# Kernel tuning notes

Measured on AMD Instinct MI355X. Metric: run time of the kernel, lower is better.

Reference implementation:

```python
import jax, jax.numpy as jnp
import numpy as np
from jax import lax

B, T, MELS, H, K = 32, 2048, 80, 128, 5
MAX_WORDS, MAX_DUR = 64, 128


def _conv1d(x, w, b):
    # x: [B,C,T], w: [O,I,K]
    y = lax.conv_general_dilated(x, w, (1,), 'SAME',
                                 dimension_numbers=('NCH', 'OIH', 'NCH'))
    return y + b[None, :, None]


def _conv2d(x, w, b):
    # x: [B,C,H,W], w: [O,I,K,K]
    y = lax.conv_general_dilated(x, w, (1, 1), 'SAME',
                                 dimension_numbers=('NCHW', 'OIHW', 'NCHW'))
    return y + b[None, :, None, None]


def setup_inputs() -> dict:
    key = jax.random.key(0)
    ks = jax.random.split(key, 20)
    features = jax.random.normal(ks[0], (B, MELS, T), dtype=jnp.float32)
    # monotone word boundaries in [0, T]; starts = bnds[:, :-1], ends = bnds[:, 1:]
    bnds = jnp.sort(jax.random.randint(ks[1], (B, MAX_WORDS + 1), 0, T), axis=-1)
    word_bounds = jnp.stack([bnds[:, :-1], bnds[:, 1:]], axis=1).astype(jnp.int64)  # [B,2,W]
    word_lengths = jax.random.randint(ks[2], (B,), MAX_WORDS // 2, MAX_WORDS + 1).astype(jnp.int64)
    s = 0.05
    p = {
        'w1': jax.random.normal(ks[3], (H, MELS, K)) * s, 'b1': jnp.zeros((H,)),
        'w2': jax.random.normal(ks[4], (H, H, K)) * s, 'b2': jnp.zeros((H,)),
        'w3': jax.random.normal(ks[5], (H, H, K)) * s, 'b3': jnp.zeros((H,)),
        'cw1': jax.random.normal(ks[6], (H, H, K, K)) * s, 'cb1': jnp.zeros((H,)),
        'cw2': jax.random.normal(ks[7], (H, H, K, K)) * s, 'cb2': jnp.zeros((H,)),
        'lw': jax.random.normal(ks[8], (1, MAX_DUR)) * s, 'lb': jnp.zeros((1,)),
        'cw3': jax.random.normal(ks[9], (1, H, K, K)) * s, 'cb3': jnp.zeros((1,)),
    }
    return {'features': features, 'word_bounds': word_bounds, 'word_lengths': word_lengths, **p}


def _slice_words(emb, word_bounds, word_lengths):
    # emb: [B,H,T] -> padded [B,H,MAX_WORDS,MAX_DUR]
    starts = word_bounds[:, 0, :]                      # [B,W]
    durs = word_bounds[:, 1, :] - starts               # [B,W]
    j = jnp.arange(MAX_DUR)                            # [D]
    idx = starts[:, :, None] + j[None, None, :]        # [B,W,D]
    valid = (j[None, None, :] < durs[:, :, None]) & \
            (jnp.arange(MAX_WORDS)[None, :, None] < word_lengths[:, None, None])
    idx = jnp.clip(idx, 0, emb.shape[-1] - 1)
    gathered = jax.vmap(lambda e, ix: e[:, ix])(emb, idx)  # [B,H,W,D]
    return gathered * valid[:, None, :, :].astype(emb.dtype)


def reference(features, word_bounds, word_lengths,
              w1, b1, w2, b2, w3, b3,
              cw1, cb1, cw2, cb2, lw, lb, cw3, cb3):
    # frame encoder
    x = jax.nn.relu(_conv1d(features, w1, b1))
    x = jax.nn.relu(_conv1d(x, w2, b2))
    emb = _conv1d(x, w3, b3)                           # [B,H,T]
    # ragged word slicing + zero-pad scatter (vectorized gather)
    padded = _slice_words(emb, word_bounds, word_lengths)  # [B,H,W,D]
    # word decoder
    y = jax.nn.relu(_conv2d(padded, cw1, cb1))
    y = jax.nn.relu(_conv2d(y, cw2, cb2))
    y = jax.nn.relu(jnp.einsum('bcwd,od->bcwo', y, lw) + lb)  # Linear over duration dim
    out = _conv2d(y, cw3, cb3)                         # [B,1,W,1]
    return out
```

## Files before the change

kernel.cpp:

```cpp
#include <hip/hip_runtime.h>
#include <hip/hip_bf16.h>

#define BB 32
#define TT 2048
#define MELS 80
#define HH 128
#define WW 64
#define DD 128

using bf16x8 = __attribute__((ext_vector_type(8))) short;
using f32x16 = __attribute__((ext_vector_type(16))) float;
using u16x4  = __attribute__((ext_vector_type(4))) ushort;

#define MFMA(av, bv, acc) acc = __builtin_amdgcn_mfma_f32_32x32x16_bf16(av, bv, acc, 0, 0, 0)

__device__ __forceinline__ ushort bf16b(float f) {
  __hip_bfloat16 h = __float2bfloat16(f);
  return *(ushort*)&h;
}

__device__ __forceinline__ void g2l16(const ushort* g, ushort* l) {
  __builtin_amdgcn_global_load_lds((const __attribute__((address_space(1))) void*)g,
                                   (__attribute__((address_space(3))) void*)l, 16, 0, 0);
}

__device__ __forceinline__ void dump_tile(const f32x16& a, int tl, int mb, int half,
                                          const float* __restrict__ bias, bool relu,
                                          ushort* s_y) {
  #pragma unroll
  for (int q = 0; q < 4; ++q) {
    int ho0 = mb + 8 * q + 4 * half;
    u16x4 p;
    #pragma unroll
    for (int j = 0; j < 4; ++j) {
      float v = a[q * 4 + j] + bias[ho0 + j];
      if (relu) v = fmaxf(v, 0.f);
      p[j] = bf16b(v);
    }
    *(u16x4*)&s_y[tl * 128 + (((ho0 >> 3) ^ (tl & 15)) << 3) + (ho0 & 7)] = p;
  }
}

__global__ __launch_bounds__(256) void prep_all(
    const float* __restrict__ features,
    const float* __restrict__ w1, const float* __restrict__ w2,
    const float* __restrict__ w3, const float* __restrict__ cw1,
    const float* __restrict__ cw2, const float* __restrict__ cb1,
    const float* __restrict__ lw,
    ushort* __restrict__ ft, ushort* __restrict__ Wb1, ushort* __restrict__ Wb2,
    ushort* __restrict__ Wb3, ushort* __restrict__ Wc1, ushort* __restrict__ Wc2,
    float* __restrict__ T2, float* __restrict__ Ls, ushort* __restrict__ zp) {
  __shared__ float s[MELS][65];
  const int bb = blockIdx.x, tid = threadIdx.x;
  if (bb < 1024) {
    const int b = bb >> 5, t0 = (bb & 31) * 64;
    for (int i = tid; i < MELS * 64; i += 256) {
      int c = i >> 6, t = i & 63;
      s[c][t] = features[(b * MELS + c) * TT + t0 + t];
    }
    __syncthreads();
    for (int i = tid; i < 64 * 128; i += 256) {
      int t = i >> 7, c = i & 127;
      float v = (c < MELS) ? s[c][t] : 0.f;
      ft[(b * TT + t0 + t) * 128 + c] = bf16b(v);
    }
  } else if (bb < 1864) {
    int rel, NSS, C; const float* w; ushort* Wb;
    if (bb < 1224)      { rel = bb - 1024; NSS = 5; C = MELS; w = w1; Wb = Wb1; }
    else if (bb < 1544) { rel = bb - 1224; NSS = 8; C = HH;   w = w2; Wb = Wb2; }
    else                { rel = bb - 1544; NSS = 8; C = HH;   w = w3; Wb = Wb3; }
    int i = rel * 256 + tid;
    int e = i & 7, m = (i >> 3) & 127, half = (i >> 10) & 1;
    int r = i >> 11;
    int ss = r % NSS, kw = r / NSS;
    int c = ss * 16 + half * 8 + e;
    Wb[i] = bf16b(w[(m * C + c) * 5 + kw]);
  } else if (bb < 5064) {
    int rel; const float* cw; ushort* Wc;
    if (bb < 3464) { rel = bb - 1864; cw = cw1; Wc = Wc1; }
    else           { rel = bb - 3464; cw = cw2; Wc = Wc2; }
    int i = rel * 256 + tid;
    int e = i & 7, m = (i >> 3) & 127, half = (i >> 10) & 1, ss = (i >> 11) & 7;
    int r = i >> 14;
    int kw = r % 5, kd = r / 5;
    int hi = ss * 16 + half * 8 + e;
    Wc[i] = bf16b(cw[((m * HH + hi) * 5 + kw) * 5 + kd]);
  } else if (bb < 5067) {
    int i = (bb - 5064) * 256 + tid;
    if (i < 640) {
      int ho = i / 5, kw = i - ho * 5;
      float sA = 0.f, sB = 0.f, sC = 0.f;
      for (int hi = 0; hi < HH; ++hi) {
        float yc = fmaxf(cb1[hi], 0.f);
        const float* p = cw2 + ((ho * HH + hi) * 5 + kw) * 5;
        float c012 = p[0] + p[1] + p[2];
        sC += c012 * yc;
        sB += (c012 + p[3]) * yc;
        sA += (c012 + p[3] + p[4]) * yc;
      }
      T2[i * 3 + 0] = sA; T2[i * 3 + 1] = sB; T2[i * 3 + 2] = sC;
    } else if (i < 645) {
      int c = i - 640;
      float sv = 0.f;
      for (int d = c * 32; d < 128; ++d) sv += lw[d];
      Ls[c] = sv;
    }
  } else {
    *(bf16x8*)(zp + tid * 8) = (short)0;
  }
}

template<int NSS, int RELU>
__global__ __launch_bounds__(256) void conv1d_mfma(
    const ushort* __restrict__ xt, const ushort* __restrict__ Wb,
    const float* __restrict__ bias, ushort* __restrict__ yt,
    const ushort* __restrict__ zp) {
  __shared__ __align__(16) ushort s_x[1088 * 8];
  const int bid = blockIdx.x;
  const int nid = (bid & 7) * 128 + (bid >> 3);
  const int b = nid >> 5;
  const int t0 = (nid & 31) << 6;
  const int tid = threadIdx.x;
  const int lane = tid & 63, wv = tid >> 6;
  const int l31 = lane & 31, half = lane >> 5;
  const int m_w = (wv >> 1) * 64, n32 = (wv & 1) * 32;

  #pragma unroll
  for (int it = 0; it < 5; ++it) {
    int slot = it * 256 + tid;
    if (slot < 1088) {
      int row = slot >> 4, bsw = (slot & 15) ^ (row & 15);
      int t = t0 + row - 2;
      const ushort* src = ((unsigned)t < TT)
          ? xt + (((size_t)(b * TT + t)) << 7) + bsw * 8 : zp;
      g2l16(src, s_x + slot * 8);
    }
  }
  __syncthreads();

  f32x16 a0 = 0.f, a1 = 0.f;
  const bf16x8* Ap = (const bf16x8*)Wb;
  constexpr int G = 5 * NSS;
  #pragma unroll
  for (int g = 0; g < G; ++g) {
    const int kw = g / NSS, ss = g % NSS;
    int r0 = n32 + l31 + kw;
    int blk = ss * 2 + half;
    bf16x8 bv = *(const bf16x8*)&s_x[r0 * 128 + ((blk ^ (r0 & 15)) << 3)];
    int ai = ((kw * NSS + ss) * 2 + half) * 128 + m_w + l31;
    MFMA(Ap[ai],      bv, a0);
    MFMA(Ap[ai + 32], bv, a1);
  }
  __syncthreads();
  dump_tile(a0, n32 + l31, m_w,      half, bias, RELU != 0, s_x);
  dump_tile(a1, n32 + l31, m_w + 32, half, bias, RELU != 0, s_x);
  __syncthreads();
  #pragma unroll
  for (int it = 0; it < 4; ++it) {
    int i = it * 256 + tid;
    int tl = i >> 4, blk = i & 15;
    bf16x8 v = *(const bf16x8*)&s_x[tl * 128 + ((blk ^ (tl & 15)) << 3)];
    *(bf16x8*)(yt + (((size_t)(b * TT + t0 + tl)) << 7) + blk * 8) = v;
  }
}

#define COMPUTE2D(KW, BUF, NB)                                                 \
  {                                                                            \
    bf16x8 ar[2][8];                                                           \
    _Pragma("unroll")                                                          \
    for (int j = 0; j < 8; ++j)                                                \
      ar[0][j] = Ap[(((0 * 5 + (KW)) * 8 + (j >> 1)) * 2 + half) * 128 +       \
                    m_w + l31 + (j & 1) * 32];                                 \
    __builtin_amdgcn_s_setprio(1);                                             \
    _Pragma("unroll")                                                          \
    for (int g = 0; g < 10; ++g) {                                             \
      int kd = g >> 1, sh = (g & 1) * 4;                                       \
      if (g < 9) {                                                             \
        int kd2 = (g + 1) >> 1, sh2 = ((g + 1) & 1) * 4;                       \
        _Pragma("unroll")                                                      \
        for (int j = 0; j < 8; ++j)                                            \
          ar[(g + 1) & 1][j] = Ap[(((kd2 * 5 + (KW)) * 8 + sh2 + (j >> 1)) * 2 \
                                   + half) * 128 + m_w + l31 + (j & 1) * 32];  \
      }                                                                        \
      _Pragma("unroll")                                                        \
      for (int s2 = 0; s2 < 4; ++s2) {                                         \
        int ss = sh + s2;                                                      \
        int r0 = n_w + l31 + kd;                                               \
        int blk = ss * 2 + half;                                               \
        bf16x8 bv0 = *(const bf16x8*)&(BUF)[r0 * 128 + ((blk ^ (r0 & 15)) << 3)]; \
        MFMA(ar[g & 1][s2 * 2],     bv0, a00);                                 \
        MFMA(ar[g & 1][s2 * 2 + 1], bv0, a10);                                 \
        if ((NB) > 1) {                                                        \
          int r1 = r0 + 32;                                                    \
          bf16x8 bv1 = *(const bf16x8*)&(BUF)[r1 * 128 + ((blk ^ (r1 & 15)) << 3)]; \
          MFMA(ar[g & 1][s2 * 2],     bv1, a01);                               \
          MFMA(ar[g & 1][s2 * 2 + 1], bv1, a11);                               \
        }                                                                      \
      }                                                                        \
    }                                                                          \
    __builtin_amdgcn_s_setprio(0);                                             \
  }

__global__ __launch_bounds__(256, 4) void conv2d1_mfma(
    const ushort* __restrict__ embt, const int* __restrict__ wb,
    const int* __restrict__ wlen, const ushort* __restrict__ Wc,
    const float* __restrict__ cb, ushort* __restrict__ y1t,
    const ushort* __restrict__ zp) {
  extern __shared__ __align__(16) ushort smem[];
  const int bid = blockIdx.x;
  const int nid = (bid & 7) * 256 + (bid >> 3);
  const int b = nid >> 6, w = nid & 63;
  const int tid = threadIdx.x;
  const int lane = tid & 63, wv = tid >> 6;
  const int l31 = lane & 31, half = lane >> 5;
  const int m_w = (wv >> 1) * 64, n_w = (wv & 1) * 64;

  int stv[5], duv[5];
  const int wl = wlen[b];
  #pragma unroll
  for (int i = 0; i < 5; ++i) {
    int wq = w + i - 2;
    bool ok = ((unsigned)wq < WW) && (wq < wl);
    int st = ok ? wb[b * 128 + wq] : 0;
    int en = ok ? wb[b * 128 + 64 + wq] : 0;
    stv[i] = st;
    duv[i] = ok ? min(en - st, 128) : 0;
  }
  int dcap = 0;
  #pragma unroll
  for (int i = 0; i < 5; ++i) dcap = max(dcap, duv[i]);
  const int NT1 = min(4, max(1, (dcap + 2 + 31) >> 5));
  const int rstage = min(132, NT1 * 32 + 4);
  const int t0a = n_w >> 5;
  const bool act0 = t0a < NT1, act1 = t0a + 1 < NT1;

#define STAGE1(KW)                                                             \
  {                                                                            \
    const int st_ = stv[KW], du_ = duv[KW];                                    \
    if (du_ > 0) {                                                             \
      const int rs_ = min(rstage, (((du_ + 33) >> 5) << 5) + 4);               \
      _Pragma("unroll")                                                        \
      for (int it = 0; it < 9; ++it) {                                         \
        int slot = it * 256 + tid;                                             \
        if (slot < 2112) {                                                     \
          int row = slot >> 4;                                                 \
          if (row < rs_) {                                                     \
            int bsw = (slot & 15) ^ (row & 15);                                \
            int dq = row - 2;                                                  \
            const ushort* src = ((unsigned)dq < (unsigned)du_)                 \
                ? embt + (((size_t)(b * TT + st_ + dq)) << 7) + bsw * 8 : zp;  \
            g2l16(src, smem + slot * 8);                                       \
          }                                                                    \
        }                                                                      \
      }                                                                        \
    }                                                                          \
  }

  f32x16 a00 = 0.f, a01 = 0.f, a10 = 0.f, a11 = 0.f;
  const bf16x8* Ap = (const bf16x8*)Wc;

  STAGE1(0);
  __syncthreads();
  #pragma unroll
  for (int kw = 0; kw < 5; ++kw) {
    const int du = duv[kw];
    const bool a1k = act1 && (du + 2 > n_w + 32);
    const bool a0k = act0 && (du > 0) && (du + 2 > n_w);
    if (a1k)      { COMPUTE2D(kw, smem, 2); }
    else if (a0k) { COMPUTE2D(kw, smem, 1); }
    __syncthreads();
    if (kw < 4) {
      switch (kw + 1) {
        case 1: STAGE1(1); break;
        case 2: STAGE1(2); break;
        case 3: STAGE1(3); break;
        case 4: STAGE1(4); break;
      }
      __syncthreads();
    }
  }
#undef STAGE1

  if (act0) {
    dump_tile(a00, n_w + l31, m_w,      half, cb, true, smem);
    dump_tile(a10, n_w + l31, m_w + 32, half, cb, true, smem);
  }
  if (act1) {
    dump_tile(a01, n_w + 32 + l31, m_w,      half, cb, true, smem);
    dump_tile(a11, n_w + 32 + l31, m_w + 32, half, cb, true, smem);
  }
  __syncthreads();
  bf16x8 cv;
  {
    int blkc = tid & 15;
    #pragma unroll
    for (int j = 0; j < 8; ++j)
      ((ushort*)&cv)[j] = bf16b(fmaxf(cb[blkc * 8 + j], 0.f));
  }
  #pragma unroll
  for (int it = 0; it < 8; ++it) {
    int i = it * 256 + tid;
    int d = i >> 4, blk = i & 15;
    bf16x8 v = (d < NT1 * 32)
        ? *(const bf16x8*)&smem[d * 128 + ((blk ^ (d & 15)) << 3)] : cv;
    *(bf16x8*)(y1t + (((size_t)(b * WW + w) * DD + d) << 7) + blk * 8) = v;
  }
}

__global__ __launch_bounds__(256, 4) void conv2d2_mfma(
    const ushort* __restrict__ y1t, const int* __restrict__ wb,
    const int* __restrict__ wlen, const ushort* __restrict__ Wc,
    const float* __restrict__ cb, const float* __restrict__ lw,
    const float* __restrict__ lb, const float* __restrict__ T2,
    const float* __restrict__ Ls, float* __restrict__ z,
    const ushort* __restrict__ zp) {
  extern __shared__ __align__(16) ushort smem[];
  const int bid = blockIdx.x;
  const int nid = (bid & 7) * 256 + (bid >> 3);
  const int b = nid >> 6, w = nid & 63;
  const int tid = threadIdx.x;
  const int lane = tid & 63, wv = tid >> 6;
  const int l31 = lane & 31, half = lane >> 5;
  const int m_w = (wv >> 1) * 64, n_w = (wv & 1) * 64;

  int dmax = 0;
  const int wl = wlen[b];
  #pragma unroll
  for (int i = 0; i < 9; ++i) {
    int wq = w + i - 4;
    if ((unsigned)wq < WW && wq < wl) {
      int du = min(wb[b * 128 + 64 + wq] - wb[b * 128 + wq], 128);
      dmax = max(dmax, du);
    }
  }
  const int NT2 = min(4, max(1, (dmax + 4 + 31) >> 5));
  const int rstage = min(132, NT2 * 32 + 4);
  const int t0a = n_w >> 5;
  const bool act0 = t0a < NT2, act1 = t0a + 1 < NT2;

#define STAGE2(KW)                                                             \
  {                                                                            \
    const int wq_ = w + (KW) - 2;                                              \
    if ((unsigned)wq_ < WW) {                                                  \
      _Pragma("unroll")                                                        \
      for (int it = 0; it < 9; ++it) {                                         \
        int slot = it * 256 + tid;                                             \
        if (slot < 2112) {                                                     \
          int row = slot >> 4;                                                 \
          if (row < rstage) {                                                  \
            int bsw = (slot & 15) ^ (row & 15);                                \
            int dq = row - 2;                                                  \
            const ushort* src = ((unsigned)dq < (unsigned)DD)                  \
                ? y1t + (((size_t)(b * WW + wq_) * DD + dq) << 7) + bsw * 8 : zp;\
            g2l16(src, smem + slot * 8);                                       \
          }                                                                    \
        }                                                                      \
      }                                                                        \
    }                                                                          \
  }

  f32x16 a00 = 0.f, a01 = 0.f, a10 = 0.f, a11 = 0.f;
  const bf16x8* Ap = (const bf16x8*)Wc;

  STAGE2(0);
  __syncthreads();
  #pragma unroll
  for (int kw = 0; kw < 5; ++kw) {
    const bool kok = (unsigned)(w + kw - 2) < WW;
    if (kok && act1)      { COMPUTE2D(kw, smem, 2); }
    else if (kok && act0) { COMPUTE2D(kw, smem, 1); }
    __syncthreads();
    if (kw < 4) {
      switch (kw + 1) {
        case 1: STAGE2(1); break;
        case 2: STAGE2(2); break;
        case 3: STAGE2(3); break;
        case 4: STAGE2(4); break;
      }
      __syncthreads();
    }
  }
#undef STAGE2

  float* s_red = (float*)smem;
  const float lw0 = lw[n_w + l31], lw1 = lw[n_w + 32 + l31];
  #pragma unroll
  for (int r = 0; r < 16; ++r) {
    int rowoff = (r & 3) + 8 * (r >> 2) + 4 * half;
    {
      int ho = m_w + rowoff;
      float c = cb[ho];
      float v = (act0 ? fmaxf(a00[r] + c, 0.f) * lw0 : 0.f)
              + (act1 ? fmaxf(a01[r] + c, 0.f) * lw1 : 0.f);
      v += __shfl_xor(v, 1); v += __shfl_xor(v, 2); v += __shfl_xor(v, 4);
      v += __shfl_xor(v, 8); v += __shfl_xor(v, 16);
      if (l31 == 0) s_red[ho * 2 + (wv & 1)] = v;
    }
    {
      int ho = m_w + 32 + rowoff;
      float c = cb[ho];
      float v = (act0 ? fmaxf(a10[r] + c, 0.f) * lw0 : 0.f)
              + (act1 ? fmaxf(a11[r] + c, 0.f) * lw1 : 0.f);
      v += __shfl_xor(v, 1); v += __shfl_xor(v, 2); v += __shfl_xor(v, 4);
      v += __shfl_xor(v, 8); v += __shfl_xor(v, 16);
      if (l31 == 0) s_red[ho * 2 + (wv & 1)] = v;
    }
  }
  __syncthreads();
  if (tid < HH) {
    int ho = tid;
    float hiv = 0.f;
    if (NT2 < 4) {
      float ccA = 0.f, ccB = 0.f, ccC = 0.f;
      #pragma unroll
      for (int kw = 0; kw < 5; ++kw) {
        int wq = w + kw - 2;
        if ((unsigned)wq < WW) {
          ccA += T2[(ho * 5 + kw) * 3 + 0];
          ccB += T2[(ho * 5 + kw) * 3 + 1];
          ccC += T2[(ho * 5 + kw) * 3 + 2];
        }
      }
      float c = cb[ho];
      float l126 = lw[126], l127 = lw[127];
      hiv = fmaxf(ccA + c, 0.f) * (Ls[NT2] - l126 - l127)
          + fmaxf(ccB + c, 0.f) * l126
          + fmaxf(ccC + c, 0.f) * l127;
    }
    float zz = fmaxf(s_red[ho * 2] + s_red[ho * 2 + 1] + hiv + lb[0], 0.f);
    z[(b * HH + ho) * WW + w] = zz;
  }
}

__global__ __launch_bounds__(256) void final_k(const float* __restrict__ z,
        const float* __restrict__ cw3, const float* __restrict__ cb3,
        float* __restrict__ out) {
  __shared__ float sred[4][64];
  const int b = blockIdx.x;
  const int tid = threadIdx.x;
  const int w = tid & 63, g = tid >> 6;
  float acc = 0.f;
  for (int hi = g * 32; hi < g * 32 + 32; ++hi) {
    const float* zp_ = z + (b * HH + hi) * WW;
    const float* cp = cw3 + hi * 25 + 2;
    #pragma unroll
    for (int kw = 0; kw < 5; ++kw) {
      int ww = w + kw - 2;
      if ((unsigned)ww < WW) acc += cp[kw * 5] * zp_[ww];
    }
  }
  sred[g][w] = acc;
  __syncthreads();
  if (tid < 64)
    out[b * WW + w] = cb3[0] + sred[0][w] + sred[1][w] + sred[2][w] + sred[3][w];
}

extern "C" void kernel_launch(void* const* d_in, const int* in_sizes, int n_in,
                              void* d_out, int out_size, void* d_ws, size_t ws_size,
                              hipStream_t stream) {
  const float* features = (const float*)d_in[0];
  const int*   wbnd     = (const int*)d_in[1];
  const int*   wlen     = (const int*)d_in[2];
  const float* w1  = (const float*)d_in[3];
  const float* b1  = (const float*)d_in[4];
  const float* w2  = (const float*)d_in[5];
  const float* b2  = (const float*)d_in[6];
  const float* w3  = (const float*)d_in[7];
  const float* b3  = (const float*)d_in[8];
  const float* cw1 = (const float*)d_in[9];
  const float* cb1 = (const float*)d_in[10];
  const float* cw2 = (const float*)d_in[11];
  const float* cb2 = (const float*)d_in[12];
  const float* lw  = (const float*)d_in[13];
  const float* lb  = (const float*)d_in[14];
  const float* cw3 = (const float*)d_in[15];
  const float* cb3 = (const float*)d_in[16];
  float* out = (float*)d_out;

  char* ws = (char*)d_ws;
  ushort* ft   = (ushort*)(ws + 0);
  ushort* x1t  = (ushort*)(ws + 16777216);
  ushort* x2t  = (ushort*)(ws + 33554432);
  ushort* embt = (ushort*)(ws + 0);
  ushort* y1t  = (ushort*)(ws + 16777216);
  float*  z    = (float*)(ws + 83886080);
  ushort* Wb1  = (ushort*)(ws + 84934656);
  ushort* Wb2  = (ushort*)(ws + 85037056);
  ushort* Wb3  = (ushort*)(ws + 85200896);
  ushort* Wc1  = (ushort*)(ws + 85364736);
  ushort* Wc2  = (ushort*)(ws + 86183936);
  ushort* zp   = (ushort*)(ws + 87003136);
  float*  T2   = (float*)(ws + 87007232);
  float*  Ls   = (float*)(ws + 87014912);

  const int DYN = 16896 * 2;
  hipFuncSetAttribute((const void*)conv2d1_mfma,
                      hipFuncAttributeMaxDynamicSharedMemorySize, DYN);
  hipFuncSetAttribute((const void*)conv2d2_mfma,
                      hipFuncAttributeMaxDynamicSharedMemorySize, DYN);

  prep_all<<<5068, 256, 0, stream>>>(features, w1, w2, w3, cw1, cw2, cb1, lw,
                                     ft, Wb1, Wb2, Wb3, Wc1, Wc2, T2, Ls, zp);
  conv1d_mfma<5, 1><<<1024, 256, 0, stream>>>(ft, Wb1, b1, x1t, zp);
  conv1d_mfma<8, 1><<<1024, 256, 0, stream>>>(x1t, Wb2, b2, x2t, zp);
  conv1d_mfma<8, 0><<<1024, 256, 0, stream>>>(x2t, Wb3, b3, embt, zp);
  conv2d1_mfma<<<BB * WW, 256, DYN, stream>>>(embt, wbnd, wlen, Wc1, cb1, y1t, zp);
  conv2d2_mfma<<<BB * WW, 256, DYN, stream>>>(y1t, wbnd, wlen, Wc2, cb2, lw, lb,
                                              T2, Ls, z, zp);
  final_k<<<BB, 256, 0, stream>>>(z, cw3, cb3, out);
}
```

Measured before the change: 341.6 us.

## Skip conv1d tiles outside word span and avoid writing constant y1 padding rows

The three conv1d kernels now exit early for time tiles that lie outside the range covered by any word (widened by the remaining receptive-field halo), so frames no later stage reads are never computed. conv2d1 no longer writes the constant relu(bias) rows beyond each word's active duration. Instead conv2d2 stages those rows from a small precomputed bias vector, chosen per kw from the neighbouring word durations. This removes compute and global write/read traffic, at the cost of leaving stale data in unused parts of the workspace and relying on correct halo bookkeeping.

Result: faster. 331.1 us (-3.1%).

```diff
diff --git a/kernel.cpp b/kernel.cpp
--- a/kernel.cpp
+++ b/kernel.cpp
@@ -49,7 +49,8 @@
     const float* __restrict__ lw,
     ushort* __restrict__ ft, ushort* __restrict__ Wb1, ushort* __restrict__ Wb2,
     ushort* __restrict__ Wb3, ushort* __restrict__ Wc1, ushort* __restrict__ Wc2,
-    float* __restrict__ T2, float* __restrict__ Ls, ushort* __restrict__ zp) {
+    float* __restrict__ T2, float* __restrict__ Ls, ushort* __restrict__ zp,
+    ushort* __restrict__ cvp) {
   __shared__ float s[MELS][65];
   const int bb = blockIdx.x, tid = threadIdx.x;
   if (bb < 1024) {
@@ -107,19 +108,25 @@
     }
   } else {
     *(bf16x8*)(zp + tid * 8) = (short)0;
-  }
-}
-
-template<int NSS, int RELU>
+    if (tid < 128) cvp[tid] = bf16b(fmaxf(cb1[tid], 0.f));
+  }
+}
+
+template<int NSS, int RELU, int D>
 __global__ __launch_bounds__(256) void conv1d_mfma(
     const ushort* __restrict__ xt, const ushort* __restrict__ Wb,
     const float* __restrict__ bias, ushort* __restrict__ yt,
-    const ushort* __restrict__ zp) {
+    const ushort* __restrict__ zp, const int* __restrict__ wb,
+    const int* __restrict__ wlen) {
   __shared__ __align__(16) ushort s_x[1088 * 8];
   const int bid = blockIdx.x;
   const int nid = (bid & 7) * 128 + (bid >> 3);
   const int b = nid >> 5;
   const int t0 = (nid & 31) << 6;
+  const int wlb = wlen[b];
+  const int lo = wb[b * 128];
+  const int hi = wb[b * 128 + 64 + wlb - 1];
+  if (t0 >= hi + D || t0 + 64 <= lo - D) return;
   const int tid = threadIdx.x;
   const int lane = tid & 63, wv = tid >> 6;
   const int l31 = lane & 31, half = lane >> 5;
@@ -290,20 +297,14 @@
     dump_tile(a11, n_w + 32 + l31, m_w + 32, half, cb, true, smem);
   }
   __syncthreads();
-  bf16x8 cv;
-  {
-    int blkc = tid & 15;
-    #pragma unroll
-    for (int j = 0; j < 8; ++j)
-      ((ushort*)&cv)[j] = bf16b(fmaxf(cb[blkc * 8 + j], 0.f));
-  }
   #pragma unroll
   for (int it = 0; it < 8; ++it) {
     int i = it * 256 + tid;
     int d = i >> 4, blk = i & 15;
-    bf16x8 v = (d < NT1 * 32)
-        ? *(const bf16x8*)&smem[d * 128 + ((blk ^ (d & 15)) << 3)] : cv;
-    *(bf16x8*)(y1t + (((size_t)(b * WW + w) * DD + d) << 7) + blk * 8) = v;
+    if (d < NT1 * 32) {
+      bf16x8 v = *(const bf16x8*)&smem[d * 128 + ((blk ^ (d & 15)) << 3)];
+      *(bf16x8*)(y1t + (((size_t)(b * WW + w) * DD + d) << 7) + blk * 8) = v;
+    }
   }
 }
 
@@ -313,7 +314,7 @@
     const float* __restrict__ cb, const float* __restrict__ lw,
     const float* __restrict__ lb, const float* __restrict__ T2,
     const float* __restrict__ Ls, float* __restrict__ z,
-    const ushort* __restrict__ zp) {
+    const ushort* __restrict__ zp, const ushort* __restrict__ cvp) {
   extern __shared__ __align__(16) ushort smem[];
   const int bid = blockIdx.x;
   const int nid = (bid & 7) * 256 + (bid >> 3);
@@ -323,15 +324,17 @@
   const int l31 = lane & 31, half = lane >> 5;
   const int m_w = (wv >> 1) * 64, n_w = (wv & 1) * 64;
 
+  int duq[9];
   int dmax = 0;
   const int wl = wlen[b];
   #pragma unroll
   for (int i = 0; i < 9; ++i) {
     int wq = w + i - 4;
-    if ((unsigned)wq < WW && wq < wl) {
-      int du = min(wb[b * 128 + 64 + wq] - wb[b * 128 + wq], 128);
-      dmax = max(dmax, du);
-    }
+    int du = 0;
+    if ((unsigned)wq < WW && wq < wl)
+      du = min(wb[b * 128 + 64 + wq] - wb[b * 128 + wq], 128);
+    duq[i] = du;
+    dmax = max(dmax, du);
   }
   const int NT2 = min(4, max(1, (dmax + 4 + 31) >> 5));
   const int rstage = min(132, NT2 * 32 + 4);
@@ -342,6 +345,10 @@
   {                                                                            \
     const int wq_ = w + (KW) - 2;                                              \
     if ((unsigned)wq_ < WW) {                                                  \
+      int dc_ = 0;                                                             \
+      _Pragma("unroll")                                                        \
+      for (int m5 = 0; m5 < 5; ++m5) dc_ = max(dc_, duq[(KW) + m5]);           \
+      const int lim_ = min(4, max(1, (dc_ + 33) >> 5)) << 5;   \
       _Pragma("unroll")                                                        \
       for (int it = 0; it < 9; ++it) {                                         \
         int slot = it * 256 + tid;                                             \
@@ -350,8 +357,13 @@
           if (row < rstage) {                                                  \
             int bsw = (slot & 15) ^ (row & 15);                                \
             int dq = row - 2;                                                  \
-            const ushort* src = ((unsigned)dq < (unsigned)DD)                  \
-                ? y1t + (((size_t)(b * WW + wq_) * DD + dq) << 7) + bsw * 8 : zp;\
+            const ushort* src;                                                 \
+            if ((unsigned)dq < (unsigned)lim_)                                 \
+              src = y1t + (((size_t)(b * WW + wq_) * DD + dq) << 7) + bsw * 8; \
+            else if ((unsigned)dq < (unsigned)DD)                              \
+              src = cvp + bsw * 8;                                             \
+            else                                                               \
+              src = zp;                                                        \
             g2l16(src, smem + slot * 8);                                       \
           }                                                                    \
         }                                                                      \
@@ -492,6 +504,7 @@
   ushort* zp   = (ushort*)(ws + 87003136);
   float*  T2   = (float*)(ws + 87007232);
   float*  Ls   = (float*)(ws + 87014912);
+  ushort* cvp  = (ushort*)(ws + 87015424);
 
   const int DYN = 16896 * 2;
   hipFuncSetAttribute((const void*)conv2d1_mfma,
@@ -500,12 +513,12 @@
                       hipFuncAttributeMaxDynamicSharedMemorySize, DYN);
 
   prep_all<<<5068, 256, 0, stream>>>(features, w1, w2, w3, cw1, cw2, cb1, lw,
-                                     ft, Wb1, Wb2, Wb3, Wc1, Wc2, T2, Ls, zp);
-  conv1d_mfma<5, 1><<<1024, 256, 0, stream>>>(ft, Wb1, b1, x1t, zp);
-  conv1d_mfma<8, 1><<<1024, 256, 0, stream>>>(x1t, Wb2, b2, x2t, zp);
-  conv1d_mfma<8, 0><<<1024, 256, 0, stream>>>(x2t, Wb3, b3, embt, zp);
+                                     ft, Wb1, Wb2, Wb3, Wc1, Wc2, T2, Ls, zp, cvp);
+  conv1d_mfma<5, 1, 4><<<1024, 256, 0, stream>>>(ft, Wb1, b1, x1t, zp, wbnd, wlen);
+  conv1d_mfma<8, 1, 2><<<1024, 256, 0, stream>>>(x1t, Wb2, b2, x2t, zp, wbnd, wlen);
+  conv1d_mfma<8, 0, 0><<<1024, 256, 0, stream>>>(x2t, Wb3, b3, embt, zp, wbnd, wlen);
   conv2d1_mfma<<<BB * WW, 256, DYN, stream>>>(embt, wbnd, wlen, Wc1, cb1, y1t, zp);
   conv2d2_mfma<<<BB * WW, 256, DYN, stream>>>(y1t, wbnd, wlen, Wc2, cb2, lw, lb,
-                                              T2, Ls, z, zp);
+                                              T2, Ls, z, zp, cvp);
   final_k<<<BB, 256, 0, stream>>>(z, cw3, cb3, out);
 }
```
